# Kernel optimization log

Measured on AMD Instinct MI355X. Metric: run time of the kernel, lower is better.

## Reference

```python
import jax, jax.numpy as jnp
import numpy as np

N = 50000      # nodes
E = 1600000    # edges (avg degree 32)
F_IN = 512     # in_channels
H = 128        # hidden_channels


def setup_inputs() -> dict:
    key = jax.random.key(0)
    k0, k1, k2, k3 = jax.random.split(key, 4)
    x = jax.random.normal(k0, (N, F_IN), dtype=jnp.float32)
    edge_index = jax.random.randint(k1, (2, E), 0, N, dtype=jnp.int32)
    edge_weight = jnp.ones((E,), dtype=jnp.float32)
    # GCNConv weight (glorot) + bias, Linear weight (xavier) + bias.
    # Stored as [in, out] for direct matmul (same math as torch's x @ W.T).
    W_conv = jax.random.normal(k2, (F_IN, H), dtype=jnp.float32) * np.sqrt(2.0 / (F_IN + H)).astype(np.float32)
    b_conv = jnp.zeros((H,), dtype=jnp.float32)
    W_lin = jax.random.normal(k3, (H, F_IN), dtype=jnp.float32) * np.sqrt(2.0 / (H + F_IN)).astype(np.float32)
    b_lin = jnp.zeros((F_IN,), dtype=jnp.float32)
    return {
        "x": x, "edge_index": edge_index, "edge_weight": edge_weight,
        "W_conv": W_conv, "b_conv": b_conv, "W_lin": W_lin, "b_lin": b_lin,
    }


def reference(x, edge_index, edge_weight, W_conv, b_conv, W_lin, b_lin):
    n = x.shape[0]
    src, dst = edge_index[0], edge_index[1]
    # GCN normalization with self-loops (add_self_loops + sym norm)
    loop = jnp.arange(n, dtype=edge_index.dtype)
    src_f = jnp.concatenate([src, loop])            # [E+N]
    dst_f = jnp.concatenate([dst, loop])
    w = jnp.concatenate([edge_weight, jnp.ones((n,), x.dtype)])
    deg = jax.ops.segment_sum(w, dst_f, num_segments=n)  # [N]
    dinv = jnp.where(deg > 0, jax.lax.rsqrt(deg), 0.0)
    norm = dinv[src_f] * w * dinv[dst_f]            # [E+N]
    # GCNConv: transform then normalized neighbor aggregation
    h = x @ W_conv                                  # [N, H]
    agg = jax.ops.segment_sum(h[src_f] * norm[:, None], dst_f, num_segments=n) + b_conv  # [N, H]
    # dropout p=0.0 (eval) is identity; final linear projection back to F_IN
    return agg @ W_lin + b_lin                      # [N, F_IN]
```

## Files before the change

### kernel.cpp

```cpp
#include <hip/hip_runtime.h>

#define NN 50000
#define EE 1600000
#define FIN 512
#define HH 128

#define CAP 80
#define OVF_CAP 64512

#define GROUP 128
#define NB ((NN + GROUP - 1) / GROUP)
#define NBLK 256
#define EPB (EE / NBLK)

typedef short s16x8 __attribute__((ext_vector_type(8)));
typedef float f32x4 __attribute__((ext_vector_type(4)));

static __device__ inline unsigned short f2bf(float f) {
    unsigned u = __float_as_uint(f);
    unsigned r = (u + 0x7fffu + ((u >> 16) & 1u)) >> 16;
    return (unsigned short)r;
}

static __device__ inline float blo(unsigned u) { return __uint_as_float(u << 16); }
static __device__ inline float bhi(unsigned u) { return __uint_as_float(u & 0xffff0000u); }

static __device__ inline float deg2dinv(float d) { return (d > 0.0f) ? rsqrtf(d) : 0.0f; }


__global__ __launch_bounds__(256) void hist_kernel(const int* __restrict__ dst,
                                                   int* __restrict__ hist) {
    __shared__ int h[NB];
    const int tid = threadIdx.x;
    for (int i = tid; i < NB; i += 256) h[i] = 0;
    __syncthreads();
    const int base = blockIdx.x * EPB;
    for (int i = tid; i < EPB; i += 256)
        atomicAdd(&h[dst[base + i] >> 7], 1);
    __syncthreads();
    for (int i = tid; i < NB; i += 256) hist[blockIdx.x * NB + i] = h[i];
}

__global__ __launch_bounds__(64) void scan_bins(const int* __restrict__ hist,
                                                int* __restrict__ off,
                                                int* __restrict__ binTotal) {
    const int bin = blockIdx.x;
    const int lane = threadIdx.x;
    int v[4];
    int s = 0;
#pragma unroll
    for (int i = 0; i < 4; ++i) { v[i] = hist[(lane * 4 + i) * NB + bin]; s += v[i]; }
    int incl = s;
#pragma unroll
    for (int d = 1; d < 64; d <<= 1) {
        int t = __shfl_up(incl, d, 64);
        if (lane >= d) incl += t;
    }
    int run = incl - s;
#pragma unroll
    for (int i = 0; i < 4; ++i) { off[(lane * 4 + i) * NB + bin] = run; run += v[i]; }
    if (lane == 63) binTotal[bin] = incl;
}

__global__ __launch_bounds__(512) void bin_base(const int* __restrict__ binTotal,
                                                int* __restrict__ binBase) {
    __shared__ int s[512];
    const int t = threadIdx.x;
    int mine = (t < NB) ? binTotal[t] : 0;
    s[t] = mine;
    __syncthreads();
    for (int d = 1; d < 512; d <<= 1) {
        int v = (t >= d) ? s[t - d] : 0;
        __syncthreads();
        s[t] += v;
        __syncthreads();
    }
    if (t < NB) binBase[t] = s[t] - mine;
}

__global__ __launch_bounds__(256) void place_kernel(const int* __restrict__ src,
                                                    const int* __restrict__ dst,
                                                    const float* __restrict__ w,
                                                    const int* __restrict__ off,
                                                    const int* __restrict__ binBase,
                                                    int2* __restrict__ bins) {
    __shared__ int cur[NB];
    const int tid = threadIdx.x;
    for (int i = tid; i < NB; i += 256)
        cur[i] = binBase[i] + off[blockIdx.x * NB + i];
    __syncthreads();
    const int base = blockIdx.x * EPB;
    for (int i = tid; i < EPB; i += 256) {
        int e = base + i;
        int s = src[e], d = dst[e];
        float we = w[e];
        int pos = atomicAdd(&cur[d >> 7], 1);
        bins[pos] = make_int2(s | ((d & 127) << 16), __float_as_int(we));
    }
}

__global__ __launch_bounds__(512) void bucket_build(const int* __restrict__ binBase,
                                                    const int* __restrict__ binTotal,
                                                    const int2* __restrict__ bins,
                                                    int* __restrict__ cnt,
                                                    int2* __restrict__ bucket,
                                                    float* __restrict__ deg,
                                                    int* __restrict__ ovf_cnt,
                                                    int4* __restrict__ ovf) {
    __shared__ int lcnt[GROUP];
    __shared__ float lw[GROUP];
    const int b = blockIdx.x;
    const int tid = threadIdx.x;
    if (tid < GROUP) { lcnt[tid] = 0; lw[tid] = 0.0f; }
    __syncthreads();
    const int base = b * GROUP;
    const int start = binBase[b];
    const int n = binTotal[b];
    for (int i = tid; i < n; i += 512) {
        int2 en = bins[start + i];
        int sr = en.x & 0xffff;
        int dl = (en.x >> 16) & 127;
        int pos = atomicAdd(&lcnt[dl], 1);
        if (pos < CAP) {
            bucket[(size_t)(base + dl) * CAP + pos] = make_int2(sr, en.y);
            atomicAdd(&lw[dl], __int_as_float(en.y));
        } else {
            int o = atomicAdd(ovf_cnt, 1);
            if (o < OVF_CAP) ovf[o] = make_int4(sr, base + dl, en.y, 0);
        }
    }
    __syncthreads();
    for (int i = tid; i < GROUP; i += 512) {
        int node = base + i;
        if (node < NN) {
            cnt[node] = lcnt[i];
            deg[node] = 1.0f + lw[i];
        }
    }
}

__global__ void ovf_deg(const int* __restrict__ ovf_cnt, const int4* __restrict__ ovf,
                        float* __restrict__ deg) {
    int n = min(*ovf_cnt, OVF_CAP);
    for (int i = blockIdx.x * blockDim.x + threadIdx.x; i < n; i += blockDim.x * gridDim.x)
        atomicAdd(deg + ovf[i].y, __int_as_float(ovf[i].z));
}


__global__ __launch_bounds__(512) void gemm1_kernel(const float* __restrict__ A,
                                                    const float* __restrict__ B,
                                                    const float* __restrict__ deg,
                                                    unsigned short* __restrict__ h2,
                                                    int M) {
    __shared__ short As[128][40];
    __shared__ short Bs[128][40];
    const int bm = blockIdx.x * 128;
    const int tid = threadIdx.x;
    const int wave = tid >> 6, lane = tid & 63;
    const int wm = wave >> 1, wn = wave & 1;
    const int mlane = lane & 15, quad = lane >> 4;

    const int ar = tid >> 3, akq = tid & 7;
    const int bn = tid & 127, bkg = tid >> 7;

    f32x4 acc[2][4];
#pragma unroll
    for (int i = 0; i < 2; ++i)
#pragma unroll
        for (int j = 0; j < 4; ++j) acc[i][j] = (f32x4){0.f, 0.f, 0.f, 0.f};

    float4 pa0[2], pa1[2];
    float pb0[8], pb1[8];

    auto loadT = [&](float4 (&pa)[2], float (&pb)[8], int k0) {
#pragma unroll
        for (int i = 0; i < 2; ++i) {
            int grow = bm + ar + i * 64;
            pa[i] = make_float4(0.f, 0.f, 0.f, 0.f);
            if (grow < M) pa[i] = *(const float4*)(A + (size_t)grow * FIN + k0 + akq * 4);
        }
#pragma unroll
        for (int j = 0; j < 8; ++j)
            pb[j] = B[(size_t)(k0 + bkg * 8 + j) * HH + bn];
    };
    auto storeT = [&](float4 (&pa)[2], float (&pb)[8]) {
#pragma unroll
        for (int i = 0; i < 2; ++i) {
            ushort4 b;
            b.x = f2bf(pa[i].x); b.y = f2bf(pa[i].y); b.z = f2bf(pa[i].z); b.w = f2bf(pa[i].w);
            *(ushort4*)&As[ar + i * 64][akq * 4] = b;
        }
        unsigned short tmp[8];
#pragma unroll
        for (int j = 0; j < 8; ++j) tmp[j] = f2bf(pb[j]);
        *(s16x8*)&Bs[bn][bkg * 8] = *(s16x8*)tmp;
    };
    auto mmaT = [&]() {
        s16x8 af[2], bfr[4];
#pragma unroll
        for (int mt = 0; mt < 2; ++mt)
            af[mt] = *(const s16x8*)&As[wm * 32 + mt * 16 + mlane][quad * 8];
#pragma unroll
        for (int nt = 0; nt < 4; ++nt)
            bfr[nt] = *(const s16x8*)&Bs[wn * 64 + nt * 16 + mlane][quad * 8];
#pragma unroll
        for (int mt = 0; mt < 2; ++mt)
#pragma unroll
            for (int nt = 0; nt < 4; ++nt)
                acc[mt][nt] = __builtin_amdgcn_mfma_f32_16x16x32_bf16(af[mt], bfr[nt], acc[mt][nt], 0, 0, 0);
    };

    loadT(pa0, pb0, 0);
    loadT(pa1, pb1, 32);
    for (int kk = 0; kk < 16; kk += 2) {
        storeT(pa0, pb0);
        __syncthreads();
        if (kk + 2 < 16) loadT(pa0, pb0, (kk + 2) * 32);
        mmaT();
        __syncthreads();
        storeT(pa1, pb1);
        __syncthreads();
        if (kk + 3 < 16) loadT(pa1, pb1, (kk + 3) * 32);
        mmaT();
        __syncthreads();
    }

#pragma unroll
    for (int mt = 0; mt < 2; ++mt) {
#pragma unroll
        for (int r = 0; r < 4; ++r) {
            int row = bm + wm * 32 + mt * 16 + quad * 4 + r;
            if (row < M) {
                float sc = deg2dinv(deg[row]);
#pragma unroll
                for (int nt = 0; nt < 4; ++nt) {
                    int col = wn * 64 + nt * 16 + mlane;
                    h2[(size_t)row * HH + col] = f2bf(acc[mt][nt][r] * sc);
                }
            }
        }
    }
}


__global__ __launch_bounds__(256) void agg_kernel(const unsigned int* __restrict__ h2u,
                                                  const int* __restrict__ cnt,
                                                  const int2* __restrict__ bucket,
                                                  const float* __restrict__ deg,
                                                  const float* __restrict__ b_conv,
                                                  const int* __restrict__ ovf_cnt,
                                                  const int4* __restrict__ ovf,
                                                  unsigned int* __restrict__ aggu, int n) {
    int idx = blockIdx.x * 256 + threadIdx.x;
    int node = idx >> 6;
    int lane = idx & 63;
    if (node >= n) return;
    int c = min(cnt[node], CAP);
    const int2* e = bucket + (size_t)node * CAP;

    unsigned self = h2u[(size_t)node * 64 + lane];
    float a0 = blo(self), a1 = bhi(self);
    float b0 = 0.0f, b1 = 0.0f;

    int j = 0;
    for (; j + 8 <= c; j += 8) {
        int4 p0 = *(const int4*)(e + j);
        int4 p1 = *(const int4*)(e + j + 2);
        int4 p2 = *(const int4*)(e + j + 4);
        int4 p3 = *(const int4*)(e + j + 6);
        unsigned u0 = h2u[(size_t)p0.x * 64 + lane];
        unsigned u1 = h2u[(size_t)p0.z * 64 + lane];
        unsigned u2 = h2u[(size_t)p1.x * 64 + lane];
        unsigned u3 = h2u[(size_t)p1.z * 64 + lane];
        unsigned u4 = h2u[(size_t)p2.x * 64 + lane];
        unsigned u5 = h2u[(size_t)p2.z * 64 + lane];
        unsigned u6 = h2u[(size_t)p3.x * 64 + lane];
        unsigned u7 = h2u[(size_t)p3.z * 64 + lane];
        float w0 = __int_as_float(p0.y), w1 = __int_as_float(p0.w);
        float w2 = __int_as_float(p1.y), w3 = __int_as_float(p1.w);
        float w4 = __int_as_float(p2.y), w5 = __int_as_float(p2.w);
        float w6 = __int_as_float(p3.y), w7 = __int_as_float(p3.w);
        a0 += w0 * blo(u0); a1 += w0 * bhi(u0);
        b0 += w1 * blo(u1); b1 += w1 * bhi(u1);
        a0 += w2 * blo(u2); a1 += w2 * bhi(u2);
        b0 += w3 * blo(u3); b1 += w3 * bhi(u3);
        a0 += w4 * blo(u4); a1 += w4 * bhi(u4);
        b0 += w5 * blo(u5); b1 += w5 * bhi(u5);
        a0 += w6 * blo(u6); a1 += w6 * bhi(u6);
        b0 += w7 * blo(u7); b1 += w7 * bhi(u7);
    }
    for (; j + 2 <= c; j += 2) {
        int4 p = *(const int4*)(e + j);
        unsigned u0 = h2u[(size_t)p.x * 64 + lane];
        unsigned u1 = h2u[(size_t)p.z * 64 + lane];
        float w0 = __int_as_float(p.y), w1 = __int_as_float(p.w);
        a0 += w0 * blo(u0); a1 += w0 * bhi(u0);
        b0 += w1 * blo(u1); b1 += w1 * bhi(u1);
    }
    if (j < c) {
        int2 p = e[j];
        float w0 = __int_as_float(p.y);
        unsigned u0 = h2u[(size_t)p.x * 64 + lane];
        a0 += w0 * blo(u0); a1 += w0 * bhi(u0);
    }

    int ovf_n = min(*ovf_cnt, OVF_CAP);
    for (int i = 0; i < ovf_n; ++i) {
        int4 v = ovf[i];
        if (v.y == node) {
            float w0 = __int_as_float(v.z);
            unsigned u0 = h2u[(size_t)v.x * 64 + lane];
            a0 += w0 * blo(u0); a1 += w0 * bhi(u0);
        }
    }

    float di = deg2dinv(deg[node]);
    float2 bc = *(const float2*)&b_conv[lane * 2];
    float v0 = bc.x + di * (a0 + b0);
    float v1 = bc.y + di * (a1 + b1);
    aggu[(size_t)node * 64 + lane] = (unsigned)f2bf(v0) | ((unsigned)f2bf(v1) << 16);
}


__global__ __launch_bounds__(512) void gemm2_kernel(const unsigned short* __restrict__ A,
                                                    const float* __restrict__ B,
                                                    const float* __restrict__ bias,
                                                    float* __restrict__ C,
                                                    int M) {
    __shared__ short As[128][40];
    __shared__ short Bs[128][40];
    const int bm = blockIdx.x * 128;
    const int bnb = blockIdx.y * 128;
    const int tid = threadIdx.x;
    const int wave = tid >> 6, lane = tid & 63;
    const int wm = wave >> 1, wn = wave & 1;
    const int mlane = lane & 15, quad = lane >> 4;

    const int ar = tid >> 2, ach = tid & 3;
    const int bn = tid & 127, bkg = tid >> 7;

    f32x4 acc[2][4];
#pragma unroll
    for (int i = 0; i < 2; ++i)
#pragma unroll
        for (int j = 0; j < 4; ++j) acc[i][j] = (f32x4){0.f, 0.f, 0.f, 0.f};

    s16x8 pa0, pa1;
    float pb0[8], pb1[8];

    auto loadT = [&](s16x8& pa, float (&pb)[8], int k0) {
        int grow = bm + ar;
        pa = (s16x8){0, 0, 0, 0, 0, 0, 0, 0};
        if (grow < M) pa = *(const s16x8*)(A + (size_t)grow * HH + k0 + ach * 8);
#pragma unroll
        for (int j = 0; j < 8; ++j)
            pb[j] = B[(size_t)(k0 + bkg * 8 + j) * FIN + bnb + bn];
    };
    auto storeT = [&](s16x8& pa, float (&pb)[8]) {
        *(s16x8*)&As[ar][ach * 8] = pa;
        unsigned short tmp[8];
#pragma unroll
        for (int j = 0; j < 8; ++j) tmp[j] = f2bf(pb[j]);
        *(s16x8*)&Bs[bn][bkg * 8] = *(s16x8*)tmp;
    };
    auto mmaT = [&]() {
        s16x8 af[2], bfr[4];
#pragma unroll
        for (int mt = 0; mt < 2; ++mt)
            af[mt] = *(const s16x8*)&As[wm * 32 + mt * 16 + mlane][quad * 8];
#pragma unroll
        for (int nt = 0; nt < 4; ++nt)
            bfr[nt] = *(const s16x8*)&Bs[wn * 64 + nt * 16 + mlane][quad * 8];
#pragma unroll
        for (int mt = 0; mt < 2; ++mt)
#pragma unroll
            for (int nt = 0; nt < 4; ++nt)
                acc[mt][nt] = __builtin_amdgcn_mfma_f32_16x16x32_bf16(af[mt], bfr[nt], acc[mt][nt], 0, 0, 0);
    };

    loadT(pa0, pb0, 0);
    loadT(pa1, pb1, 32);
    for (int kk = 0; kk < 4; kk += 2) {
        storeT(pa0, pb0);
        __syncthreads();
        if (kk + 2 < 4) loadT(pa0, pb0, (kk + 2) * 32);
        mmaT();
        __syncthreads();
        storeT(pa1, pb1);
        __syncthreads();
        if (kk + 3 < 4) loadT(pa1, pb1, (kk + 3) * 32);
        mmaT();
        __syncthreads();
    }

#pragma unroll
    for (int mt = 0; mt < 2; ++mt) {
#pragma unroll
        for (int r = 0; r < 4; ++r) {
            int row = bm + wm * 32 + mt * 16 + quad * 4 + r;
            if (row < M) {
#pragma unroll
                for (int nt = 0; nt < 4; ++nt) {
                    int col = bnb + wn * 64 + nt * 16 + mlane;
                    C[(size_t)row * FIN + col] = acc[mt][nt][r] + bias[col];
                }
            }
        }
    }
}


extern "C" void kernel_launch(void* const* d_in, const int* in_sizes, int n_in,
                              void* d_out, int out_size, void* d_ws, size_t ws_size,
                              hipStream_t stream) {
    const float* x      = (const float*)d_in[0];
    const int*   ei     = (const int*)d_in[1];
    const float* ew     = (const float*)d_in[2];
    const float* W_conv = (const float*)d_in[3];
    const float* b_conv = (const float*)d_in[4];
    const float* W_lin  = (const float*)d_in[5];
    const float* b_lin  = (const float*)d_in[6];
    float* out = (float*)d_out;

    const int* src = ei;
    const int* dst = ei + EE;

    char* ws = (char*)d_ws;
    int*            cnt      = (int*)           (ws + 0);
    float*          deg      = (float*)         (ws + 200704);
    int*            ovf_cnt  = (int*)           (ws + 602112);
    int*            binTotal = (int*)           (ws + 602368);
    int*            binBase  = (int*)           (ws + 604160);
    int4*           ovf      = (int4*)          (ws + 605952);
    int2*           bucket   = (int2*)          (ws + 1650944);
    unsigned short* h2       = (unsigned short*)(ws + 33650944);
    unsigned short* agg      = (unsigned short*)(ws + 46450944);

    int*            hist     = (int*)           (ws + 1650944);
    int*            off      = (int*)           (ws + 2051584);
    int2*           bins     = (int2*)          (ws + 33650944);

    hipMemsetAsync(ovf_cnt, 0, sizeof(int), stream);

    const int nb_w = (NN * 64 + 255) / 256;

    hist_kernel<<<NBLK, 256, 0, stream>>>(dst, hist);
    scan_bins<<<NB, 64, 0, stream>>>(hist, off, binTotal);
    bin_base<<<1, 512, 0, stream>>>(binTotal, binBase);
    place_kernel<<<NBLK, 256, 0, stream>>>(src, dst, ew, off, binBase, bins);
    bucket_build<<<NB, 512, 0, stream>>>(binBase, binTotal, bins, cnt, bucket, deg, ovf_cnt, ovf);
    ovf_deg<<<4, 256, 0, stream>>>(ovf_cnt, ovf, deg);

    gemm1_kernel<<<dim3((NN + 127) / 128, 1), 512, 0, stream>>>(x, W_conv, deg, h2, NN);

    agg_kernel<<<nb_w, 256, 0, stream>>>((const unsigned int*)h2, cnt, bucket, deg, b_conv,
                                         ovf_cnt, ovf, (unsigned int*)agg, NN);

    gemm2_kernel<<<dim3((NN + 127) / 128, FIN / 128), 512, 0, stream>>>(agg, W_lin, b_lin, out, NN);
}
```

Measured before the change: 349.1 us.

## Split aggregation into four column-slice passes and shrink gemm1 tiles

The gather-based aggregation is split into four launches, each covering a 16-lane (32-column) slice of the hidden features, with 16 nodes per block. The goal is a smaller gathered working set per pass so neighbour rows stay in cache. gemm1 drops to 64-row tiles so more blocks are launched. The bin_base and ovf_deg kernels are removed: bin bases now come from an atomic cursor in scan_bins, and degree weights are accumulated for overflowed edges too. The cost is re-reading the edge buckets four times plus extra launches, and bin order is no longer sorted by bin index.

```diff
diff --git a/kernel.cpp b/kernel.cpp
--- a/kernel.cpp
+++ b/kernel.cpp
@@ -43,7 +43,9 @@
 
 __global__ __launch_bounds__(64) void scan_bins(const int* __restrict__ hist,
                                                 int* __restrict__ off,
-                                                int* __restrict__ binTotal) {
+                                                int* __restrict__ binTotal,
+                                                int* __restrict__ binBase,
+                                                int* __restrict__ cursor) {
     const int bin = blockIdx.x;
     const int lane = threadIdx.x;
     int v[4];
@@ -59,23 +61,10 @@
     int run = incl - s;
 #pragma unroll
     for (int i = 0; i < 4; ++i) { off[(lane * 4 + i) * NB + bin] = run; run += v[i]; }
-    if (lane == 63) binTotal[bin] = incl;
-}
-
-__global__ __launch_bounds__(512) void bin_base(const int* __restrict__ binTotal,
-                                                int* __restrict__ binBase) {
-    __shared__ int s[512];
-    const int t = threadIdx.x;
-    int mine = (t < NB) ? binTotal[t] : 0;
-    s[t] = mine;
-    __syncthreads();
-    for (int d = 1; d < 512; d <<= 1) {
-        int v = (t >= d) ? s[t - d] : 0;
-        __syncthreads();
-        s[t] += v;
-        __syncthreads();
-    }
-    if (t < NB) binBase[t] = s[t] - mine;
+    if (lane == 63) {
+        binTotal[bin] = incl;
+        binBase[bin] = atomicAdd(cursor, incl);
+    }
 }
 
 __global__ __launch_bounds__(256) void place_kernel(const int* __restrict__ src,
@@ -120,10 +109,10 @@
         int2 en = bins[start + i];
         int sr = en.x & 0xffff;
         int dl = (en.x >> 16) & 127;
+        atomicAdd(&lw[dl], __int_as_float(en.y));
         int pos = atomicAdd(&lcnt[dl], 1);
         if (pos < CAP) {
             bucket[(size_t)(base + dl) * CAP + pos] = make_int2(sr, en.y);
-            atomicAdd(&lw[dl], __int_as_float(en.y));
         } else {
             int o = atomicAdd(ovf_cnt, 1);
             if (o < OVF_CAP) ovf[o] = make_int4(sr, base + dl, en.y, 0);
@@ -139,22 +128,15 @@
     }
 }
 
-__global__ void ovf_deg(const int* __restrict__ ovf_cnt, const int4* __restrict__ ovf,
-                        float* __restrict__ deg) {
-    int n = min(*ovf_cnt, OVF_CAP);
-    for (int i = blockIdx.x * blockDim.x + threadIdx.x; i < n; i += blockDim.x * gridDim.x)
-        atomicAdd(deg + ovf[i].y, __int_as_float(ovf[i].z));
-}
-
 
 __global__ __launch_bounds__(512) void gemm1_kernel(const float* __restrict__ A,
                                                     const float* __restrict__ B,
                                                     const float* __restrict__ deg,
                                                     unsigned short* __restrict__ h2,
                                                     int M) {
-    __shared__ short As[128][40];
+    __shared__ short As[64][40];
     __shared__ short Bs[128][40];
-    const int bm = blockIdx.x * 128;
+    const int bm = blockIdx.x * 64;
     const int tid = threadIdx.x;
     const int wave = tid >> 6, lane = tid & 63;
     const int wm = wave >> 1, wn = wave & 1;
@@ -163,51 +145,39 @@
     const int ar = tid >> 3, akq = tid & 7;
     const int bn = tid & 127, bkg = tid >> 7;
 
-    f32x4 acc[2][4];
-#pragma unroll
-    for (int i = 0; i < 2; ++i)
-#pragma unroll
-        for (int j = 0; j < 4; ++j) acc[i][j] = (f32x4){0.f, 0.f, 0.f, 0.f};
-
-    float4 pa0[2], pa1[2];
+    f32x4 acc[4];
+#pragma unroll
+    for (int j = 0; j < 4; ++j) acc[j] = (f32x4){0.f, 0.f, 0.f, 0.f};
+
+    float4 pa0, pa1;
     float pb0[8], pb1[8];
 
-    auto loadT = [&](float4 (&pa)[2], float (&pb)[8], int k0) {
-#pragma unroll
-        for (int i = 0; i < 2; ++i) {
-            int grow = bm + ar + i * 64;
-            pa[i] = make_float4(0.f, 0.f, 0.f, 0.f);
-            if (grow < M) pa[i] = *(const float4*)(A + (size_t)grow * FIN + k0 + akq * 4);
-        }
+    auto loadT = [&](float4& pa, float (&pb)[8], int k0) {
+        int grow = bm + ar;
+        pa = make_float4(0.f, 0.f, 0.f, 0.f);
+        if (grow < M) pa = *(const float4*)(A + (size_t)grow * FIN + k0 + akq * 4);
 #pragma unroll
         for (int j = 0; j < 8; ++j)
             pb[j] = B[(size_t)(k0 + bkg * 8 + j) * HH + bn];
     };
-    auto storeT = [&](float4 (&pa)[2], float (&pb)[8]) {
-#pragma unroll
-        for (int i = 0; i < 2; ++i) {
-            ushort4 b;
-            b.x = f2bf(pa[i].x); b.y = f2bf(pa[i].y); b.z = f2bf(pa[i].z); b.w = f2bf(pa[i].w);
-            *(ushort4*)&As[ar + i * 64][akq * 4] = b;
-        }
+    auto storeT = [&](float4& pa, float (&pb)[8]) {
+        ushort4 b;
+        b.x = f2bf(pa.x); b.y = f2bf(pa.y); b.z = f2bf(pa.z); b.w = f2bf(pa.w);
+        *(ushort4*)&As[ar][akq * 4] = b;
         unsigned short tmp[8];
 #pragma unroll
         for (int j = 0; j < 8; ++j) tmp[j] = f2bf(pb[j]);
         *(s16x8*)&Bs[bn][bkg * 8] = *(s16x8*)tmp;
     };
     auto mmaT = [&]() {
-        s16x8 af[2], bfr[4];
-#pragma unroll
-        for (int mt = 0; mt < 2; ++mt)
-            af[mt] = *(const s16x8*)&As[wm * 32 + mt * 16 + mlane][quad * 8];
+        s16x8 af, bfr[4];
+        af = *(const s16x8*)&As[wm * 16 + mlane][quad * 8];
 #pragma unroll
         for (int nt = 0; nt < 4; ++nt)
             bfr[nt] = *(const s16x8*)&Bs[wn * 64 + nt * 16 + mlane][quad * 8];
 #pragma unroll
-        for (int mt = 0; mt < 2; ++mt)
-#pragma unroll
-            for (int nt = 0; nt < 4; ++nt)
-                acc[mt][nt] = __builtin_amdgcn_mfma_f32_16x16x32_bf16(af[mt], bfr[nt], acc[mt][nt], 0, 0, 0);
+        for (int nt = 0; nt < 4; ++nt)
+            acc[nt] = __builtin_amdgcn_mfma_f32_16x16x32_bf16(af, bfr[nt], acc[nt], 0, 0, 0);
     };
 
     loadT(pa0, pb0, 0);
@@ -226,60 +196,60 @@
     }
 
 #pragma unroll
-    for (int mt = 0; mt < 2; ++mt) {
-#pragma unroll
-        for (int r = 0; r < 4; ++r) {
-            int row = bm + wm * 32 + mt * 16 + quad * 4 + r;
-            if (row < M) {
-                float sc = deg2dinv(deg[row]);
-#pragma unroll
-                for (int nt = 0; nt < 4; ++nt) {
-                    int col = wn * 64 + nt * 16 + mlane;
-                    h2[(size_t)row * HH + col] = f2bf(acc[mt][nt][r] * sc);
-                }
+    for (int r = 0; r < 4; ++r) {
+        int row = bm + wm * 16 + quad * 4 + r;
+        if (row < M) {
+            float sc = deg2dinv(deg[row]);
+#pragma unroll
+            for (int nt = 0; nt < 4; ++nt) {
+                int col = wn * 64 + nt * 16 + mlane;
+                h2[(size_t)row * HH + col] = f2bf(acc[nt][r] * sc);
             }
         }
     }
 }
 
 
-__global__ __launch_bounds__(256) void agg_kernel(const unsigned int* __restrict__ h2u,
-                                                  const int* __restrict__ cnt,
-                                                  const int2* __restrict__ bucket,
-                                                  const float* __restrict__ deg,
-                                                  const float* __restrict__ b_conv,
-                                                  const int* __restrict__ ovf_cnt,
-                                                  const int4* __restrict__ ovf,
-                                                  unsigned int* __restrict__ aggu, int n) {
-    int idx = blockIdx.x * 256 + threadIdx.x;
-    int node = idx >> 6;
-    int lane = idx & 63;
-    if (node >= n) return;
-    int c = min(cnt[node], CAP);
-    const int2* e = bucket + (size_t)node * CAP;
-
-    unsigned self = h2u[(size_t)node * 64 + lane];
-    float a0 = blo(self), a1 = bhi(self);
-    float b0 = 0.0f, b1 = 0.0f;
-
-    int j = 0;
-    for (; j + 8 <= c; j += 8) {
-        int4 p0 = *(const int4*)(e + j);
-        int4 p1 = *(const int4*)(e + j + 2);
-        int4 p2 = *(const int4*)(e + j + 4);
-        int4 p3 = *(const int4*)(e + j + 6);
-        unsigned u0 = h2u[(size_t)p0.x * 64 + lane];
-        unsigned u1 = h2u[(size_t)p0.z * 64 + lane];
-        unsigned u2 = h2u[(size_t)p1.x * 64 + lane];
-        unsigned u3 = h2u[(size_t)p1.z * 64 + lane];
-        unsigned u4 = h2u[(size_t)p2.x * 64 + lane];
-        unsigned u5 = h2u[(size_t)p2.z * 64 + lane];
-        unsigned u6 = h2u[(size_t)p3.x * 64 + lane];
-        unsigned u7 = h2u[(size_t)p3.z * 64 + lane];
-        float w0 = __int_as_float(p0.y), w1 = __int_as_float(p0.w);
-        float w2 = __int_as_float(p1.y), w3 = __int_as_float(p1.w);
-        float w4 = __int_as_float(p2.y), w5 = __int_as_float(p2.w);
-        float w6 = __int_as_float(p3.y), w7 = __int_as_float(p3.w);
+__global__ __launch_bounds__(256) void agg_pass(const unsigned int* __restrict__ h2u,
+                                                const int* __restrict__ cnt,
+                                                const int2* __restrict__ bucket,
+                                                const float* __restrict__ deg,
+                                                const float* __restrict__ b_conv,
+                                                const int* __restrict__ ovf_cnt,
+                                                const int4* __restrict__ ovf,
+                                                unsigned int* __restrict__ aggu,
+                                                int qb, int n) {
+    const int tid = threadIdx.x;
+    const int wave = tid >> 6, lane = tid & 63;
+    const int g = lane >> 4, u = lane & 15;
+    const int node = blockIdx.x * 16 + wave * 4 + g;
+    const bool valid = node < n;
+    const int c = valid ? min(cnt[node], CAP) : 0;
+    const int2* e = bucket + (size_t)(valid ? node : 0) * CAP;
+
+    float a0 = 0.f, a1 = 0.f, b0 = 0.f, b1 = 0.f;
+    for (int j = 0; j < c; j += 8) {
+        int j1 = min(j + 1, c - 1), j2 = min(j + 2, c - 1), j3 = min(j + 3, c - 1);
+        int j4 = min(j + 4, c - 1), j5 = min(j + 5, c - 1), j6 = min(j + 6, c - 1);
+        int j7 = min(j + 7, c - 1);
+        int2 p0 = e[j],  p1 = e[j1], p2 = e[j2], p3 = e[j3];
+        int2 p4 = e[j4], p5 = e[j5], p6 = e[j6], p7 = e[j7];
+        unsigned u0 = h2u[(size_t)p0.x * 64 + qb + u];
+        unsigned u1 = h2u[(size_t)p1.x * 64 + qb + u];
+        unsigned u2 = h2u[(size_t)p2.x * 64 + qb + u];
+        unsigned u3 = h2u[(size_t)p3.x * 64 + qb + u];
+        unsigned u4 = h2u[(size_t)p4.x * 64 + qb + u];
+        unsigned u5 = h2u[(size_t)p5.x * 64 + qb + u];
+        unsigned u6 = h2u[(size_t)p6.x * 64 + qb + u];
+        unsigned u7 = h2u[(size_t)p7.x * 64 + qb + u];
+        float w0 = __int_as_float(p0.y);
+        float w1 = (j + 1 < c) ? __int_as_float(p1.y) : 0.f;
+        float w2 = (j + 2 < c) ? __int_as_float(p2.y) : 0.f;
+        float w3 = (j + 3 < c) ? __int_as_float(p3.y) : 0.f;
+        float w4 = (j + 4 < c) ? __int_as_float(p4.y) : 0.f;
+        float w5 = (j + 5 < c) ? __int_as_float(p5.y) : 0.f;
+        float w6 = (j + 6 < c) ? __int_as_float(p6.y) : 0.f;
+        float w7 = (j + 7 < c) ? __int_as_float(p7.y) : 0.f;
         a0 += w0 * blo(u0); a1 += w0 * bhi(u0);
         b0 += w1 * blo(u1); b1 += w1 * bhi(u1);
         a0 += w2 * blo(u2); a1 += w2 * bhi(u2);
@@ -289,36 +259,24 @@
         a0 += w6 * blo(u6); a1 += w6 * bhi(u6);
         b0 += w7 * blo(u7); b1 += w7 * bhi(u7);
     }
-    for (; j + 2 <= c; j += 2) {
-        int4 p = *(const int4*)(e + j);
-        unsigned u0 = h2u[(size_t)p.x * 64 + lane];
-        unsigned u1 = h2u[(size_t)p.z * 64 + lane];
-        float w0 = __int_as_float(p.y), w1 = __int_as_float(p.w);
-        a0 += w0 * blo(u0); a1 += w0 * bhi(u0);
-        b0 += w1 * blo(u1); b1 += w1 * bhi(u1);
-    }
-    if (j < c) {
-        int2 p = e[j];
-        float w0 = __int_as_float(p.y);
-        unsigned u0 = h2u[(size_t)p.x * 64 + lane];
-        a0 += w0 * blo(u0); a1 += w0 * bhi(u0);
-    }
-
-    int ovf_n = min(*ovf_cnt, OVF_CAP);
-    for (int i = 0; i < ovf_n; ++i) {
-        int4 v = ovf[i];
-        if (v.y == node) {
-            float w0 = __int_as_float(v.z);
-            unsigned u0 = h2u[(size_t)v.x * 64 + lane];
-            a0 += w0 * blo(u0); a1 += w0 * bhi(u0);
+
+    if (valid) {
+        int ovf_n = min(*ovf_cnt, OVF_CAP);
+        for (int i = 0; i < ovf_n; ++i) {
+            int4 v = ovf[i];
+            if (v.y == node) {
+                float w = __int_as_float(v.z);
+                unsigned uv = h2u[(size_t)v.x * 64 + qb + u];
+                a0 += w * blo(uv); a1 += w * bhi(uv);
+            }
         }
-    }
-
-    float di = deg2dinv(deg[node]);
-    float2 bc = *(const float2*)&b_conv[lane * 2];
-    float v0 = bc.x + di * (a0 + b0);
-    float v1 = bc.y + di * (a1 + b1);
-    aggu[(size_t)node * 64 + lane] = (unsigned)f2bf(v0) | ((unsigned)f2bf(v1) << 16);
+        unsigned self = h2u[(size_t)node * 64 + qb + u];
+        float di = deg2dinv(deg[node]);
+        float2 bc = *(const float2*)&b_conv[(qb + u) * 2];
+        float v0 = bc.x + di * (blo(self) + a0 + b0);
+        float v1 = bc.y + di * (bhi(self) + a1 + b1);
+        aggu[(size_t)node * 64 + qb + u] = (unsigned)f2bf(v0) | ((unsigned)f2bf(v1) << 16);
+    }
 }
 
 
@@ -429,6 +387,7 @@
     int*            cnt      = (int*)           (ws + 0);
     float*          deg      = (float*)         (ws + 200704);
     int*            ovf_cnt  = (int*)           (ws + 602112);
+    int*            cursor   = (int*)           (ws + 602116);
     int*            binTotal = (int*)           (ws + 602368);
     int*            binBase  = (int*)           (ws + 604160);
     int4*           ovf      = (int4*)          (ws + 605952);
@@ -440,21 +399,19 @@
     int*            off      = (int*)           (ws + 2051584);
     int2*           bins     = (int2*)          (ws + 33650944);
 
-    hipMemsetAsync(ovf_cnt, 0, sizeof(int), stream);
-
-    const int nb_w = (NN * 64 + 255) / 256;
+    hipMemsetAsync(ovf_cnt, 0, 2 * sizeof(int), stream);
 
     hist_kernel<<<NBLK, 256, 0, stream>>>(dst, hist);
-    scan_bins<<<NB, 64, 0, stream>>>(hist, off, binTotal);
-    bin_base<<<1, 512, 0, stream>>>(binTotal, binBase);
+    scan_bins<<<NB, 64, 0, stream>>>(hist, off, binTotal, binBase, cursor);
     place_kernel<<<NBLK, 256, 0, stream>>>(src, dst, ew, off, binBase, bins);
     bucket_build<<<NB, 512, 0, stream>>>(binBase, binTotal, bins, cnt, bucket, deg, ovf_cnt, ovf);
-    ovf_deg<<<4, 256, 0, stream>>>(ovf_cnt, ovf, deg);
-
-    gemm1_kernel<<<dim3((NN + 127) / 128, 1), 512, 0, stream>>>(x, W_conv, deg, h2, NN);
-
-    agg_kernel<<<nb_w, 256, 0, stream>>>((const unsigned int*)h2, cnt, bucket, deg, b_conv,
-                                         ovf_cnt, ovf, (unsigned int*)agg, NN);
+
+    gemm1_kernel<<<dim3((NN + 63) / 64, 1), 512, 0, stream>>>(x, W_conv, deg, h2, NN);
+
+    const int agg_grid = (NN + 15) / 16;
+    for (int q = 0; q < 4; ++q)
+        agg_pass<<<agg_grid, 256, 0, stream>>>((const unsigned int*)h2, cnt, bucket, deg, b_conv,
+                                               ovf_cnt, ovf, (unsigned int*)agg, q * 16, NN);
 
     gemm2_kernel<<<dim3((NN + 127) / 128, FIN / 128), 512, 0, stream>>>(agg, W_lin, b_lin, out, NN);
 }
```

Measured after the change: 409.5 us. 17.3% more time.
